# Kernel tuning notes

Measured on AMD Instinct MI355X. Metric: run time of the kernel, lower is better.

## Reference

```python
import jax, jax.numpy as jnp
import numpy as np
import math

D_MODEL = 1024
NUM_HEADS = 16
D_K = D_MODEL // NUM_HEADS  # 64
B, S = 4, 2048


def setup_inputs() -> dict:
    key = jax.random.key(0)
    ks = jax.random.split(key, 9)
    sc = 1.0 / math.sqrt(D_MODEL)
    return {
        "x": jax.random.normal(ks[0], (B, S, D_MODEL), jnp.float32),
        "Wq": jax.random.normal(ks[1], (D_MODEL, D_MODEL), jnp.float32) * sc,
        "bq": jax.random.normal(ks[2], (D_MODEL,), jnp.float32) * 0.01,
        "Wk": jax.random.normal(ks[3], (D_MODEL, D_MODEL), jnp.float32) * sc,
        "bk": jax.random.normal(ks[4], (D_MODEL,), jnp.float32) * 0.01,
        "Wv": jax.random.normal(ks[5], (D_MODEL, D_MODEL), jnp.float32) * sc,
        "bv": jax.random.normal(ks[6], (D_MODEL,), jnp.float32) * 0.01,
        "Wo": jax.random.normal(ks[7], (D_MODEL, D_MODEL), jnp.float32) * sc,
        "bo": jax.random.normal(ks[8], (D_MODEL,), jnp.float32) * 0.01,
    }


def reference(x, Wq, bq, Wk, bk, Wv, bv, Wo, bo):
    b, s, d = x.shape
    # Linear projections (torch Linear: x @ W.T + b)
    Q = x @ Wq.T + bq
    K = x @ Wk.T + bk
    V = x @ Wv.T + bv
    # [b, s, h*d_k] -> [b, h, s, d_k]
    split = lambda t: t.reshape(b, s, NUM_HEADS, D_K).transpose(0, 2, 1, 3)
    Q, K, V = split(Q), split(K), split(V)
    # Causal mask: query i can attend to keys j <= i
    seq = jnp.arange(s)
    causal = seq[:, None] >= seq[None, :]  # [s, s]
    # Scaled dot-product attention
    scores = jnp.einsum('bhqd,bhkd->bhqk', Q, K) / math.sqrt(D_K)
    scores = jnp.where(causal, scores, -jnp.inf)
    weights = jax.nn.softmax(scores, axis=-1)
    attn = jnp.einsum('bhqk,bhkd->bhqd', weights, V)
    # [b, h, s, d_v] -> [b, s, h*d_v]
    attn = attn.transpose(0, 2, 1, 3).reshape(b, s, NUM_HEADS * D_K)
    return attn @ Wo.T + bo
```

## Files before the change

kernel.cpp:

```cpp
#include <hip/hip_runtime.h>
#include <hip/hip_bf16.h>


typedef unsigned short u16;
typedef unsigned int u32;
typedef __attribute__((ext_vector_type(2))) unsigned int uint2v;
typedef __attribute__((ext_vector_type(4))) unsigned int uint4v;
typedef __attribute__((ext_vector_type(4))) short short4v;
typedef __attribute__((ext_vector_type(8))) short short8;
typedef __attribute__((ext_vector_type(4))) float f32x4;
typedef __attribute__((ext_vector_type(16))) float f32x16;

#define KDIM   1024
#define S_LEN  2048
#define NHEADS 16
#define DK     64
#define NEG_BIG (-30000.0f)
#define QSCALE 0.18033688011112043f

__device__ __forceinline__ u16 f2bf(float f) {
  unsigned u = __float_as_uint(f);
  return (u16)((u + 0x7FFFu + ((u >> 16) & 1u)) >> 16);
}
__device__ __forceinline__ u32 pkbf(float a, float b) {
  u32 ua = __float_as_uint(a) + 0x8000u;
  u32 ub = __float_as_uint(b) + 0x8000u;
  return __builtin_amdgcn_perm(ub, ua, 0x07060302u);
}
__device__ __forceinline__ void gl_lds16(const u16* g, u16* l) {
  __builtin_amdgcn_global_load_lds((const __attribute__((address_space(1))) void*)g,
                                   (__attribute__((address_space(3))) void*)l, 16, 0, 0);
}

__global__ __launch_bounds__(256) void cvt_kernel(
    const float* __restrict__ x,  const float* __restrict__ Wq,
    const float* __restrict__ Wk, const float* __restrict__ Wv,
    u16* __restrict__ xb, u16* __restrict__ wqb,
    u16* __restrict__ wkb, u16* __restrict__ wvb) {
  const int NX = 2097152, NW = 262144;
  const int total = NX + 3 * NW;
  for (int i = blockIdx.x * 256 + threadIdx.x; i < total; i += gridDim.x * 256) {
    const float* src; u16* dst; int off;
    if (i < NX)               { src = x;  dst = xb;  off = i; }
    else if (i < NX + NW)     { src = Wq; dst = wqb; off = i - NX; }
    else if (i < NX + 2 * NW) { src = Wk; dst = wkb; off = i - NX - NW; }
    else                      { src = Wv; dst = wvb; off = i - NX - 2 * NW; }
    f32x4 v = *(const f32x4*)(src + (size_t)off * 4);
    short4v o;
    o[0] = (short)f2bf(v[0]); o[1] = (short)f2bf(v[1]);
    o[2] = (short)f2bf(v[2]); o[3] = (short)f2bf(v[3]);
    *(short4v*)(dst + (size_t)off * 4) = o;
  }
}

__global__ __launch_bounds__(256) void cvt_wo(const float* __restrict__ W,
                                              u16* __restrict__ out) {
  const int i = blockIdx.x * 256 + threadIdx.x;
  f32x4 v = *(const f32x4*)(W + (size_t)i * 4);
  short4v o;
  o[0] = (short)f2bf(v[0]); o[1] = (short)f2bf(v[1]);
  o[2] = (short)f2bf(v[2]); o[3] = (short)f2bf(v[3]);
  *(short4v*)(out + (size_t)i * 4) = o;
}

template <int MODE>
__device__ __forceinline__ void gemm_body(const u16* __restrict__ A,
                                          const u16* __restrict__ B,
                                          const float* __restrict__ bias,
                                          void* __restrict__ outv) {
  extern __shared__ __align__(16) u16 smem[];
  u16* As0 = smem;
  u16* As1 = smem + 4096;
  u16* Bs0 = smem + 8192;
  u16* Bs1 = smem + 12288;
  const int tid = threadIdx.x;
  const int wave = tid >> 6, lane = tid & 63;
  const int quad = lane >> 4, l16 = lane & 15;
  const int wy = wave >> 1, wx = wave & 1;
  const int m0 = blockIdx.x * 128, n0 = blockIdx.y * 128;

  f32x4 acc[4][4];
#pragma unroll
  for (int i = 0; i < 4; i++)
#pragma unroll
    for (int j = 0; j < 4; j++) acc[i][j] = (f32x4){0.f, 0.f, 0.f, 0.f};

  const int srow = wave * 16 + (lane >> 2);
  const int scol = (lane & 3) * 8;
  const u16* gA0 = A + (size_t)(m0 + srow) * KDIM + scol;
  const u16* gA1 = gA0 + (size_t)64 * KDIM;
  const u16* gB0 = B + (size_t)(n0 + srow) * KDIM + scol;
  const u16* gB1 = gB0 + (size_t)64 * KDIM;
  const int soff = srow * 32 + scol;

  for (int k = 0; k < KDIM; k += 64) {
    __syncthreads();
    gl_lds16(gA0 + k,      &As0[soff]);
    gl_lds16(gA0 + k + 32, &As1[soff]);
    gl_lds16(gA1 + k,      &As0[soff + 2048]);
    gl_lds16(gA1 + k + 32, &As1[soff + 2048]);
    gl_lds16(gB0 + k,      &Bs0[soff]);
    gl_lds16(gB0 + k + 32, &Bs1[soff]);
    gl_lds16(gB1 + k,      &Bs0[soff + 2048]);
    gl_lds16(gB1 + k + 32, &Bs1[soff + 2048]);
    __syncthreads();
#pragma unroll
    for (int h = 0; h < 2; h++) {
      const u16* Ap = h ? As1 : As0;
      const u16* Bp = h ? Bs1 : Bs0;
      short8 af[4], bfr[4];
#pragma unroll
      for (int i = 0; i < 4; i++)
        af[i] = *(const short8*)&Ap[(wy * 64 + i * 16 + l16) * 32 + quad * 8];
#pragma unroll
      for (int j = 0; j < 4; j++)
        bfr[j] = *(const short8*)&Bp[(wx * 64 + j * 16 + l16) * 32 + quad * 8];
#pragma unroll
      for (int i = 0; i < 4; i++)
#pragma unroll
        for (int j = 0; j < 4; j++) {
          if (MODE == 2)
            acc[i][j] = __builtin_amdgcn_mfma_f32_16x16x32_bf16(af[i], bfr[j], acc[i][j], 0, 0, 0);
          else
            acc[i][j] = __builtin_amdgcn_mfma_f32_16x16x32_bf16(bfr[j], af[i], acc[i][j], 0, 0, 0);
        }
    }
  }

  if (MODE == 0 || MODE == 1) {
#pragma unroll
    for (int j = 0; j < 4; j++) {
      const int colb = n0 + wx * 64 + j * 16 + quad * 4;
      const int h = colb >> 6, d0 = colb & 63;
      const f32x4 bv4 = *(const f32x4*)&bias[colb];
#pragma unroll
      for (int i = 0; i < 4; i++) {
        const int row = m0 + wy * 64 + i * 16 + l16;
        const int b = row >> 11, s = row & 2047;
        float v0 = acc[i][j][0] + bv4[0], v1 = acc[i][j][1] + bv4[1];
        float v2 = acc[i][j][2] + bv4[2], v3 = acc[i][j][3] + bv4[3];
        if (MODE == 0) { v0 *= QSCALE; v1 *= QSCALE; v2 *= QSCALE; v3 *= QSCALE; }
        uint2v pk = {pkbf(v0, v1), pkbf(v2, v3)};
        if (MODE == 0) {
          *(uint2v*)&((u16*)outv)[(((size_t)(b * NHEADS + h)) * S_LEN + s) * DK + d0] = pk;
        } else {
          *(uint2v*)&((u16*)outv)[((((size_t)(b * NHEADS + h)) * 32 + (s >> 6)) * 8 +
                                   (d0 >> 3)) * 512 + (s & 63) * 8 + (d0 & 7)] = pk;
        }
      }
    }
  } else if (MODE == 2) {
#pragma unroll
    for (int j = 0; j < 4; j++) {
      const int col = n0 + wx * 64 + j * 16 + l16;
      const int h = col >> 6, d = col & 63;
      const float bvs = bias[col];
#pragma unroll
      for (int i = 0; i < 4; i++) {
        const int rowb = m0 + wy * 64 + i * 16 + quad * 4;
        const int b = rowb >> 11, s0 = rowb & 2047;
        uint2v pk = {pkbf(acc[i][j][0] + bvs, acc[i][j][1] + bvs),
                     pkbf(acc[i][j][2] + bvs, acc[i][j][3] + bvs)};
        *(uint2v*)&((u16*)outv)[((((size_t)(b * NHEADS + h)) * 32 + (s0 >> 6)) * 8 +
                                 ((s0 >> 3) & 7)) * 512 + (size_t)d * 8 + (s0 & 7)] = pk;
      }
    }
  } else {
#pragma unroll
    for (int j = 0; j < 4; j++) {
      const int colb = n0 + wx * 64 + j * 16 + quad * 4;
      const f32x4 bv4 = *(const f32x4*)&bias[colb];
#pragma unroll
      for (int i = 0; i < 4; i++) {
        const int row = m0 + wy * 64 + i * 16 + l16;
        f32x4 v = {acc[i][j][0] + bv4[0], acc[i][j][1] + bv4[1],
                   acc[i][j][2] + bv4[2], acc[i][j][3] + bv4[3]};
        *(f32x4*)&((float*)outv)[(size_t)row * 1024 + colb] = v;
      }
    }
  }
}

__global__ __launch_bounds__(256) void qkv_gemm(
    const u16* __restrict__ xb,
    const u16* __restrict__ wqb, const float* __restrict__ bq,
    const u16* __restrict__ wkb, const float* __restrict__ bk,
    const u16* __restrict__ wvb, const float* __restrict__ bv,
    u16* __restrict__ qb, u16* __restrict__ kb, u16* __restrict__ vb) {
  if (blockIdx.z == 0)      gemm_body<0>(xb, wqb, bq, qb);
  else if (blockIdx.z == 1) gemm_body<1>(xb, wkb, bk, kb);
  else                      gemm_body<2>(xb, wvb, bv, vb);
}

__global__ __launch_bounds__(256) void out_gemm(const u16* __restrict__ A,
                                                const u16* __restrict__ wob,
                                                const float* __restrict__ bo,
                                                float* __restrict__ out) {
  gemm_body<3>(A, wob, bo, out);
}

__global__ __launch_bounds__(256) void attn_kernel(const u16* __restrict__ Qb,
                                                   const u16* __restrict__ Kb,
                                                   const u16* __restrict__ Vb,
                                                   u16* __restrict__ Ob) {
  __shared__ __align__(16) u16 Ks[2][8][512];
  __shared__ __align__(16) u16 Vs[2][8][512];
  const int bh = blockIdx.x;
  const int qt = (int)gridDim.y - 1 - (int)blockIdx.y;
  const int tid = threadIdx.x, wave = tid >> 6, lane = tid & 63;
  const int l32 = lane & 31, hi = lane >> 5;
  const u16* Qh = Qb + (size_t)bh * S_LEN * DK;
  const u16* Kg = Kb + (size_t)bh * S_LEN * DK;
  const u16* Vg = Vb + (size_t)bh * S_LEN * DK;
  const int qw = qt * 128 + wave * 32;
  const int qrow = qw + l32;

  short8 qf[4];
#pragma unroll
  for (int c = 0; c < 4; c++)
    qf[c] = *(const short8*)&Qh[(size_t)qrow * DK + c * 16 + hi * 8];

  short8 ones;
#pragma unroll
  for (int i = 0; i < 8; i++) ones[i] = (short)0x3F80;

  f32x16 zz;
#pragma unroll
  for (int i = 0; i < 16; i++) zz[i] = 0.f;
  f32x16 o0 = zz, o1 = zz, l_acc = zz;

  const int sg = wave * 2;
  const u16* srcK = Kg + sg * 512 + lane * 8;
  const u16* srcV = Vg + sg * 512 + lane * 8;
  u16* dK[2] = {&Ks[0][sg][0] + lane * 8, &Ks[1][sg][0] + lane * 8};
  u16* dV[2] = {&Vs[0][sg][0] + lane * 8, &Vs[1][sg][0] + lane * 8};

  const int nt = 2 * qt + 2;

  {
    gl_lds16(srcK, dK[0]);  gl_lds16(srcK + 512, dK[0] + 512);
    gl_lds16(srcV, dV[0]);  gl_lds16(srcV + 512, dV[0] + 512);
  }
  __syncthreads();

  int cur = 0;
  for (int t = 0; t < nt; ++t) {
    if (t + 1 < nt) {
      const size_t g = (size_t)(t + 1) * 4096;
      const int nx = cur ^ 1;
      gl_lds16(srcK + g, dK[nx]);  gl_lds16(srcK + g + 512, dK[nx] + 512);
      gl_lds16(srcV + g, dV[nx]);  gl_lds16(srcV + g + 512, dV[nx] + 512);
    }
    const u16* Kc = &Ks[cur][0][0];
    const u16* Vc = &Vs[cur][0][0];

#pragma unroll
    for (int kb = 0; kb < 2; ++kb) {
      const int kbase = t * 64 + kb * 32;
      if (kbase > qw) break;

      f32x16 st = zz;
      __builtin_amdgcn_s_setprio(1);
#pragma unroll
      for (int c = 0; c < 4; c++) {
        const short8 kf = *(const short8*)
            &Kc[(size_t)(c * 2 + hi) * 512 + (kb * 32 + l32) * 8];
        st = __builtin_amdgcn_mfma_f32_32x32x16_bf16(kf, qf[c], st, 0, 0, 0);
      }
      __builtin_amdgcn_s_setprio(0);

      if (kbase == qw) {
#pragma unroll
        for (int r = 0; r < 16; r++) {
          const int ko = (r & 3) + 8 * (r >> 2) + 4 * hi;
          st[r] = (ko > l32) ? NEG_BIG : st[r];
        }
      }

      float e[16];
#pragma unroll
      for (int r = 0; r < 16; r++) e[r] = exp2f(st[r]);

      uint2v sA0 = __builtin_amdgcn_permlane32_swap(pkbf(e[0], e[1]),  pkbf(e[4], e[5]),  false, false);
      uint2v sB0 = __builtin_amdgcn_permlane32_swap(pkbf(e[2], e[3]),  pkbf(e[6], e[7]),  false, false);
      uint2v sA1 = __builtin_amdgcn_permlane32_swap(pkbf(e[8], e[9]),  pkbf(e[12], e[13]), false, false);
      uint2v sB1 = __builtin_amdgcn_permlane32_swap(pkbf(e[10], e[11]), pkbf(e[14], e[15]), false, false);
      union { uint4v u; short8 s; } p0, p1;
      p0.u = (uint4v){sA0[0], sB0[0], sA0[1], sB0[1]};
      p1.u = (uint4v){sA1[0], sB1[0], sA1[1], sB1[1]};
      const short8 pa0 = p0.s, pa1 = p1.s;

      __builtin_amdgcn_s_setprio(1);
      l_acc = __builtin_amdgcn_mfma_f32_32x32x16_bf16(pa0, ones, l_acc, 0, 0, 0);
      l_acc = __builtin_amdgcn_mfma_f32_32x32x16_bf16(pa1, ones, l_acc, 0, 0, 0);

#pragma unroll
      for (int cc = 0; cc < 2; cc++) {
        const int kc = kb * 2 + cc;
        const short8 pa = cc ? pa1 : pa0;
        const short8 vf0 = *(const short8*)&Vc[(size_t)(kc * 2 + hi) * 512 + l32 * 8];
        const short8 vf1 = *(const short8*)&Vc[(size_t)(kc * 2 + hi) * 512 + (32 + l32) * 8];
        o0 = __builtin_amdgcn_mfma_f32_32x32x16_bf16(pa, vf0, o0, 0, 0, 0);
        o1 = __builtin_amdgcn_mfma_f32_32x32x16_bf16(pa, vf1, o1, 0, 0, 0);
      }
      __builtin_amdgcn_s_setprio(0);
    }

    if (t + 1 < nt) __syncthreads();
    cur ^= 1;
  }

  const int b = bh >> 4, h = bh & 15;
#pragma unroll
  for (int r = 0; r < 16; r++) {
    const int s = qw + (r & 3) + 8 * (r >> 2) + 4 * hi;
    const float inv = __builtin_amdgcn_rcpf(l_acc[r]);
    const unsigned v0 = __float_as_uint(o0[r] * inv) + 0x8000u;
    const unsigned v1 = __float_as_uint(o1[r] * inv) + 0x8000u;
    u16* p = &Ob[((size_t)b * S_LEN + s) * 1024 + h * DK + l32];
    p[0]  = (u16)(v0 >> 16);
    p[32] = (u16)(v1 >> 16);
  }
}

extern "C" void kernel_launch(void* const* d_in, const int* in_sizes, int n_in,
                              void* d_out, int out_size, void* d_ws, size_t ws_size,
                              hipStream_t stream) {
  const float* x  = (const float*)d_in[0];
  const float* Wq = (const float*)d_in[1];
  const float* bq = (const float*)d_in[2];
  const float* Wk = (const float*)d_in[3];
  const float* bk = (const float*)d_in[4];
  const float* Wv = (const float*)d_in[5];
  const float* bv = (const float*)d_in[6];
  const float* Wo = (const float*)d_in[7];
  const float* bo = (const float*)d_in[8];

  u16* outh = (u16*)d_out;
  u16* wsh  = (u16*)d_ws;
  u16* qb  = outh;
  u16* xb  = outh + (size_t)8388608;
  u16* kb  = wsh;
  u16* vb  = wsh + (size_t)8388608;
  u16* ab  = wsh + (size_t)16777216;
  u16* wqb = ab;
  u16* wkb = wqb + (size_t)1048576;
  u16* wvb = wkb + (size_t)1048576;
  u16* wob = kb;

  cvt_kernel<<<dim3(2048), 256, 0, stream>>>(x, Wq, Wk, Wv, xb, wqb, wkb, wvb);
  qkv_gemm<<<dim3(64, 8, 3), 256, 32768, stream>>>(xb, wqb, bq, wkb, bk, wvb, bv, qb, kb, vb);
  attn_kernel<<<dim3(64, 16), 256, 0, stream>>>(qb, kb, vb, ab);
  cvt_wo<<<dim3(1024), 256, 0, stream>>>(Wo, wob);
  out_gemm<<<dim3(64, 8), 256, 32768, stream>>>(ab, wob, bo, (float*)d_out);
}
```

Measured before the change: 257.6 us.

## Widen attention blocks to 8 waves with triple-buffered K/V prefetch

The attention kernel now uses 512-thread blocks, each covering 256 query rows, so each loaded K/V tile is shared by twice as many waves and fewer blocks are launched. The double-buffered K/V LDS ring becomes a three-deep ring that prefetches two tiles ahead and waits with explicit vmcnt counts plus a single barrier per tile instead of two syncs. Query tiles are reordered so heavy and light causal tiles are interleaved across the grid. This should cut global-load latency stalls and redundant K/V traffic, but it costs more LDS and leaves fewer, larger blocks, which can hurt occupancy and causal load balance.

Result: no change. 260.2 us (+1.0%).

```diff
diff --git a/kernel.cpp b/kernel.cpp
--- a/kernel.cpp
+++ b/kernel.cpp
@@ -199,20 +199,21 @@
   gemm_body<3>(A, wob, bo, out);
 }
 
-__global__ __launch_bounds__(256) void attn_kernel(const u16* __restrict__ Qb,
+__global__ __launch_bounds__(512) void attn_kernel(const u16* __restrict__ Qb,
                                                    const u16* __restrict__ Kb,
                                                    const u16* __restrict__ Vb,
                                                    u16* __restrict__ Ob) {
-  __shared__ __align__(16) u16 Ks[2][8][512];
-  __shared__ __align__(16) u16 Vs[2][8][512];
+  __shared__ __align__(16) u16 Ks[3][8][512];
+  __shared__ __align__(16) u16 Vs[3][8][512];
   const int bh = blockIdx.x;
-  const int qt = (int)gridDim.y - 1 - (int)blockIdx.y;
+  const int yy = blockIdx.y, half = (int)gridDim.y >> 1;
+  const int qt = (yy < half) ? ((int)gridDim.y - 1 - yy) : (yy - half);
   const int tid = threadIdx.x, wave = tid >> 6, lane = tid & 63;
   const int l32 = lane & 31, hi = lane >> 5;
   const u16* Qh = Qb + (size_t)bh * S_LEN * DK;
   const u16* Kg = Kb + (size_t)bh * S_LEN * DK;
   const u16* Vg = Vb + (size_t)bh * S_LEN * DK;
-  const int qw = qt * 128 + wave * 32;
+  const int qw = qt * 256 + wave * 32;
   const int qrow = qw + l32;
 
   short8 qf[4];
@@ -229,27 +230,28 @@
   for (int i = 0; i < 16; i++) zz[i] = 0.f;
   f32x16 o0 = zz, o1 = zz, l_acc = zz;
 
-  const int sg = wave * 2;
-  const u16* srcK = Kg + sg * 512 + lane * 8;
-  const u16* srcV = Vg + sg * 512 + lane * 8;
-  u16* dK[2] = {&Ks[0][sg][0] + lane * 8, &Ks[1][sg][0] + lane * 8};
-  u16* dV[2] = {&Vs[0][sg][0] + lane * 8, &Vs[1][sg][0] + lane * 8};
-
-  const int nt = 2 * qt + 2;
-
-  {
-    gl_lds16(srcK, dK[0]);  gl_lds16(srcK + 512, dK[0] + 512);
-    gl_lds16(srcV, dV[0]);  gl_lds16(srcV + 512, dV[0] + 512);
-  }
-  __syncthreads();
-
-  int cur = 0;
+  const u16* srcK = Kg + wave * 512 + lane * 8;
+  const u16* srcV = Vg + wave * 512 + lane * 8;
+  const int dloff = lane * 8;
+
+  const int nt = (qt + 1) * 4;
+
+  gl_lds16(srcK,        &Ks[0][wave][dloff]);
+  gl_lds16(srcV,        &Vs[0][wave][dloff]);
+  gl_lds16(srcK + 4096, &Ks[1][wave][dloff]);
+  gl_lds16(srcV + 4096, &Vs[1][wave][dloff]);
+
+  int cur = 0, pf = 2;
   for (int t = 0; t < nt; ++t) {
-    if (t + 1 < nt) {
-      const size_t g = (size_t)(t + 1) * 4096;
-      const int nx = cur ^ 1;
-      gl_lds16(srcK + g, dK[nx]);  gl_lds16(srcK + g + 512, dK[nx] + 512);
-      gl_lds16(srcV + g, dV[nx]);  gl_lds16(srcV + g + 512, dV[nx] + 512);
+    if (t + 1 < nt) asm volatile("s_waitcnt vmcnt(2)" ::: "memory");
+    else            asm volatile("s_waitcnt vmcnt(0)" ::: "memory");
+    __builtin_amdgcn_s_barrier();
+    asm volatile("" ::: "memory");
+
+    if (t + 2 < nt) {
+      const size_t g = (size_t)(t + 2) * 4096;
+      gl_lds16(srcK + g, &Ks[pf][wave][dloff]);
+      gl_lds16(srcV + g, &Vs[pf][wave][dloff]);
     }
     const u16* Kc = &Ks[cur][0][0];
     const u16* Vc = &Vs[cur][0][0];
@@ -306,8 +308,8 @@
       __builtin_amdgcn_s_setprio(0);
     }
 
-    if (t + 1 < nt) __syncthreads();
-    cur ^= 1;
+    cur = (cur == 2) ? 0 : cur + 1;
+    pf  = (pf  == 2) ? 0 : pf  + 1;
   }
 
   const int b = bh >> 4, h = bh & 15;
@@ -350,7 +352,7 @@
 
   cvt_kernel<<<dim3(2048), 256, 0, stream>>>(x, Wq, Wk, Wv, xb, wqb, wkb, wvb);
   qkv_gemm<<<dim3(64, 8, 3), 256, 32768, stream>>>(xb, wqb, bq, wkb, bk, wvb, bv, qb, kb, vb);
-  attn_kernel<<<dim3(64, 16), 256, 0, stream>>>(qb, kb, vb, ab);
+  attn_kernel<<<dim3(64, 8), 512, 0, stream>>>(qb, kb, vb, ab);
   cvt_wo<<<dim3(1024), 256, 0, stream>>>(Wo, wob);
   out_gemm<<<dim3(64, 8), 256, 32768, stream>>>(ab, wob, bo, (float*)d_out);
 }
```
